# Kernel tuning notes

Hardware: AMD Instinct MI355X
Metric: run time of the kernel (lower is better)

The kernel has to match this reference:

```python
import jax, jax.numpy as jnp
import numpy as np

DIM = 256
NUM_HEADS = 8
HEAD_DIM = DIM // NUM_HEADS          # 32
KEY_DIM = int(HEAD_DIM * 0.5)        # 16
SCALE = KEY_DIM ** (-0.5)
QKV_OUT = DIM + 2 * KEY_DIM * NUM_HEADS  # 512
BN_EPS = 1e-3


def _bn(x, gamma, beta, mean, var):
    # inference-mode BatchNorm2d over channel axis 1 of NCHW
    inv = gamma / jnp.sqrt(var + BN_EPS)
    return x * inv[None, :, None, None] + (beta - mean * inv)[None, :, None, None]


def _conv1x1(x, w):
    # w: (O, C, 1, 1)
    return jnp.einsum('bchw,oc->bohw', x, w[:, :, 0, 0])


def _dwconv3x3(x, w):
    # depthwise 3x3, SAME padding; w: (C, 1, 3, 3)
    return jax.lax.conv_general_dilated(
        x, w, window_strides=(1, 1), padding='SAME',
        feature_group_count=x.shape[1],
        dimension_numbers=('NCHW', 'OIHW', 'NCHW'))


def setup_inputs() -> dict:
    key = jax.random.key(0)
    ks = jax.random.split(key, 16)
    B, C, H, W = 16, DIM, 32, 32
    inp = {
        'x': jax.random.normal(ks[0], (B, C, H, W), jnp.float32),
        'qkv_w': jax.random.normal(ks[1], (QKV_OUT, DIM, 1, 1), jnp.float32) * (1.0 / np.sqrt(DIM)),
        'qkv_gamma': jnp.ones((QKV_OUT,), jnp.float32),
        'qkv_beta': jnp.zeros((QKV_OUT,), jnp.float32),
        'qkv_mean': jax.random.normal(ks[2], (QKV_OUT,), jnp.float32) * 0.1,
        'qkv_var': jax.random.uniform(ks[3], (QKV_OUT,), jnp.float32, 0.5, 1.5),
        'pe_w': jax.random.normal(ks[4], (DIM, 1, 3, 3), jnp.float32) * (1.0 / 3.0),
        'pe_gamma': jnp.ones((DIM,), jnp.float32),
        'pe_beta': jnp.zeros((DIM,), jnp.float32),
        'pe_mean': jax.random.normal(ks[5], (DIM,), jnp.float32) * 0.1,
        'pe_var': jax.random.uniform(ks[6], (DIM,), jnp.float32, 0.5, 1.5),
        'proj_w': jax.random.normal(ks[7], (DIM, DIM, 1, 1), jnp.float32) * (1.0 / np.sqrt(DIM)),
        'proj_gamma': jnp.ones((DIM,), jnp.float32),
        'proj_beta': jnp.zeros((DIM,), jnp.float32),
        'proj_mean': jax.random.normal(ks[8], (DIM,), jnp.float32) * 0.1,
        'proj_var': jax.random.uniform(ks[9], (DIM,), jnp.float32, 0.5, 1.5),
    }
    return inp


def reference(x, qkv_w, qkv_gamma, qkv_beta, qkv_mean, qkv_var,
              pe_w, pe_gamma, pe_beta, pe_mean, pe_var,
              proj_w, proj_gamma, proj_beta, proj_mean, proj_var):
    B, C, H, W = x.shape
    N = H * W
    # qkv: 1x1 conv + BN (act=False)
    qkv = _bn(_conv1x1(x, qkv_w), qkv_gamma, qkv_beta, qkv_mean, qkv_var)
    qkv = qkv.reshape(B, NUM_HEADS, 2 * KEY_DIM + HEAD_DIM, N)
    q = qkv[:, :, :KEY_DIM]                          # (B, h, kd, N)
    k = qkv[:, :, KEY_DIM:2 * KEY_DIM]               # (B, h, kd, N)
    v = qkv[:, :, 2 * KEY_DIM:]                      # (B, h, hd, N)
    # attn = (q^T @ k) * scale, softmax over last dim
    attn = jnp.einsum('bhdn,bhdm->bhnm', q, k) * SCALE   # (B, h, N, N)
    attn = jax.nn.softmax(attn, axis=-1)
    # v @ attn^T
    v_attn = jnp.einsum('bhdn,bhmn->bhdm', v, attn)      # (B, h, hd, N)
    v_attn = v_attn.reshape(B, C, H, W)
    v_reshaped = v.reshape(B, C, H, W)
    pos_enc = _bn(_dwconv3x3(v_reshaped, pe_w), pe_gamma, pe_beta, pe_mean, pe_var)
    out = v_attn + pos_enc
    out = _bn(_conv1x1(out, proj_w), proj_gamma, proj_beta, proj_mean, proj_var)
    return out
```

## Files before the change

kernel.cpp:

```cpp
#include <hip/hip_runtime.h>

#define B_ 16
#define C_ 256
#define N_ 1024
#define NH 8
#define HD 32
#define KD 16
#define QKV_OUT_ 512
#define BN_EPS 1e-3f
#define SCALE2_ (0.25f * 1.44269504088896f)

typedef __attribute__((ext_vector_type(8))) short short8;
typedef __attribute__((ext_vector_type(16))) float float16;

__device__ inline unsigned short f2bf(float f) {
  unsigned int u = __float_as_uint(f);
  return (unsigned short)((u + 0x7FFF + ((u >> 16) & 1)) >> 16);
}
__device__ inline float bf2f(unsigned short s) {
  return __uint_as_float(((unsigned int)s) << 16);
}
__device__ inline float16 zero16() {
  float16 z;
  #pragma unroll
  for (int i = 0; i < 16; ++i) z[i] = 0.f;
  return z;
}
__device__ inline unsigned int pack_bf16_trunc(float a, float b) {
  return __builtin_amdgcn_perm(__float_as_uint(b), __float_as_uint(a), 0x07060302u);
}
__device__ inline unsigned int pack_bf16_rne(float a, float b) {
  return (unsigned int)f2bf(a) | ((unsigned int)f2bf(b) << 16);
}
__device__ inline float fast_exp2(float x) {
#if __has_builtin(__builtin_amdgcn_exp2f)
  return __builtin_amdgcn_exp2f(x);
#else
  return exp2f(x);
#endif
}

__global__ __launch_bounds__(256) void fold_weights(
    const float* __restrict__ qkv_w, const float* __restrict__ qg,
    const float* __restrict__ qb, const float* __restrict__ qm,
    const float* __restrict__ qv,
    const float* __restrict__ proj_w, const float* __restrict__ pg,
    const float* __restrict__ pb, const float* __restrict__ pm,
    const float* __restrict__ pv,
    unsigned short* __restrict__ wq, float* __restrict__ biasq,
    unsigned short* __restrict__ wp, float* __restrict__ biasp)
{
  const int o = blockIdx.x, c = threadIdx.x;
  if (o < QKV_OUT_) {
    float inv = qg[o] * rsqrtf(qv[o] + BN_EPS);
    wq[o * C_ + c] = f2bf(qkv_w[o * C_ + c] * inv);
    if (c == 0) biasq[o] = qb[o] - qm[o] * inv;
  } else {
    int oo = o - QKV_OUT_;
    float inv = pg[oo] * rsqrtf(pv[oo] + BN_EPS);
    wp[oo * C_ + c] = f2bf(proj_w[oo * C_ + c] * inv);
    if (c == 0) biasp[oo] = pb[oo] - pm[oo] * inv;
  }
}

__global__ __launch_bounds__(256) void transpose_x(
    const float* __restrict__ x, unsigned short* __restrict__ xT)
{
  __shared__ float t[64][69];
  const int tid = threadIdx.x;
  const int nt = blockIdx.x, ct = blockIdx.y, b = blockIdx.z;
  const int n0 = nt * 64, c0 = ct * 64;

  #pragma unroll
  for (int it = 0; it < 4; ++it) {
    int cl = it * 16 + (tid >> 4);
    int nl = (tid & 15) * 4;
    float4 v = *(const float4*)(x + ((size_t)b * C_ + c0 + cl) * N_ + n0 + nl);
    t[cl][nl + 0] = v.x; t[cl][nl + 1] = v.y;
    t[cl][nl + 2] = v.z; t[cl][nl + 3] = v.w;
  }
  __syncthreads();

  const int nr = tid >> 2, cseg = (tid & 3) * 16;
  unsigned int pk[8];
  #pragma unroll
  for (int q = 0; q < 8; ++q)
    pk[q] = pack_bf16_rne(t[cseg + 2 * q][nr], t[cseg + 2 * q + 1][nr]);
  unsigned short* row = xT + ((size_t)b * N_ + n0 + nr) * C_ + c0 + cseg;
  *(uint4*)(row)     = make_uint4(pk[0], pk[1], pk[2], pk[3]);
  *(uint4*)(row + 8) = make_uint4(pk[4], pk[5], pk[6], pk[7]);
}

template <int MODE>
__global__ __launch_bounds__(256) void gemm_tiled(
    const unsigned short* __restrict__ inT, const unsigned short* __restrict__ wfold,
    const float* __restrict__ bias,
    unsigned short* __restrict__ qkT, unsigned short* __restrict__ vbuf,
    float* __restrict__ outf)
{
  __shared__ __align__(16) unsigned short wa[128 * 72];
  __shared__ __align__(16) unsigned short xb[128 * 72];
  const int tid = threadIdx.x;
  const int wave = tid >> 6, lane = tid & 63, l31 = lane & 31, lh = lane >> 5;
  const int wm = wave & 1, wn = wave >> 1;
  const int n0g = blockIdx.x * 128;
  const int o0 = blockIdx.y * 128;
  const int b = n0g >> 10, nloc = n0g & 1023;

  const int sr = tid >> 3, sseg = (tid & 7) * 8;

  float16 acc[2][2];
  #pragma unroll
  for (int i = 0; i < 2; ++i)
    #pragma unroll
    for (int j = 0; j < 2; ++j) acc[i][j] = zero16();

  for (int kc = 0; kc < 4; ++kc) {
    __syncthreads();
    #pragma unroll
    for (int rr = 0; rr < 4; ++rr) {
      int r = rr * 32 + sr;
      *(uint4*)&wa[r * 72 + sseg] =
          *(const uint4*)(wfold + (size_t)(o0 + r) * C_ + kc * 64 + sseg);
      *(uint4*)&xb[r * 72 + sseg] =
          *(const uint4*)(inT + (size_t)(n0g + r) * C_ + kc * 64 + sseg);
    }
    __syncthreads();

    #pragma unroll
    for (int ks = 0; ks < 4; ++ks) {
      const int ko = ks * 16 + lh * 8;
      short8 a0 = *(const short8*)&wa[(wm * 64 + l31) * 72 + ko];
      short8 a1 = *(const short8*)&wa[(wm * 64 + 32 + l31) * 72 + ko];
      short8 b0 = *(const short8*)&xb[(wn * 64 + l31) * 72 + ko];
      short8 b1 = *(const short8*)&xb[(wn * 64 + 32 + l31) * 72 + ko];
      acc[0][0] = __builtin_amdgcn_mfma_f32_32x32x16_bf16(a0, b0, acc[0][0], 0, 0, 0);
      acc[0][1] = __builtin_amdgcn_mfma_f32_32x32x16_bf16(a0, b1, acc[0][1], 0, 0, 0);
      acc[1][0] = __builtin_amdgcn_mfma_f32_32x32x16_bf16(a1, b0, acc[1][0], 0, 0, 0);
      acc[1][1] = __builtin_amdgcn_mfma_f32_32x32x16_bf16(a1, b1, acc[1][1], 0, 0, 0);
    }
  }

  if constexpr (MODE == 0) {
    const int h = (o0 >> 6) + wm * 2 ;
    const int hh = (o0 >> 6) + wm;
    (void)h;
    #pragma unroll
    for (int bn = 0; bn < 2; ++bn) {
      int n = nloc + wn * 64 + bn * 32 + l31;
      unsigned short* row = qkT + (((size_t)b * NH + hh) * N_ + n) * 32;
      #pragma unroll
      for (int qd = 0; qd < 4; ++qd) {
        int cc0 = 8 * qd + 4 * lh;
        ushort4 rv;
        rv.x = f2bf(acc[0][bn][4 * qd + 0] + bias[hh * 64 + cc0 + 0]);
        rv.y = f2bf(acc[0][bn][4 * qd + 1] + bias[hh * 64 + cc0 + 1]);
        rv.z = f2bf(acc[0][bn][4 * qd + 2] + bias[hh * 64 + cc0 + 2]);
        rv.w = f2bf(acc[0][bn][4 * qd + 3] + bias[hh * 64 + cc0 + 3]);
        *(ushort4*)(row + cc0) = rv;
      }
    }
    #pragma unroll
    for (int r = 0; r < 16; ++r) {
      int d = (r & 3) + 8 * (r >> 2) + 4 * lh;
      float bo = bias[hh * 64 + 32 + d];
      unsigned short* vrow =
          vbuf + ((size_t)b * C_ + hh * 32 + d) * N_ + nloc + wn * 64 + l31;
      #pragma unroll
      for (int bn = 0; bn < 2; ++bn)
        vrow[bn * 32] = f2bf(acc[1][bn][r] + bo);
    }
  } else {
    #pragma unroll
    for (int am = 0; am < 2; ++am) {
      #pragma unroll
      for (int r = 0; r < 16; ++r) {
        int o = o0 + wm * 64 + am * 32 + (r & 3) + 8 * (r >> 2) + 4 * lh;
        float bo = bias[o];
        float* orow = outf + ((size_t)b * C_ + o) * N_ + nloc + wn * 64 + l31;
        #pragma unroll
        for (int bn = 0; bn < 2; ++bn)
          orow[bn * 32] = acc[am][bn][r] + bo;
      }
    }
  }
}

__global__ __launch_bounds__(256) void dwconv_bn(
    const unsigned short* __restrict__ vbuf, const float* __restrict__ pw,
    const float* __restrict__ gamma, const float* __restrict__ beta,
    const float* __restrict__ mean, const float* __restrict__ var,
    float* __restrict__ posenc)
{
  __shared__ float t[34][34];
  const int c = blockIdx.x, b = blockIdx.y;
  const int tid = threadIdx.x;
  const unsigned short* vp = vbuf + ((size_t)b * C_ + c) * N_;

  #pragma unroll
  for (int r = 0; r < 4; ++r) {
    int idx = r * 256 + tid;
    t[(idx >> 5) + 1][(idx & 31) + 1] = bf2f(vp[idx]);
  }
  if (tid < 34) {
    t[0][tid] = 0.f; t[33][tid] = 0.f;
    t[tid][0] = 0.f; t[tid][33] = 0.f;
  }
  __syncthreads();

  float w9[9];
  #pragma unroll
  for (int i = 0; i < 9; ++i) w9[i] = pw[c * 9 + i];
  float inv = gamma[c] * rsqrtf(var[c] + BN_EPS);
  float add = beta[c] - mean[c] * inv;

  float* op = posenc + ((size_t)b * C_ + c) * N_;
  #pragma unroll
  for (int r = 0; r < 4; ++r) {
    int idx = r * 256 + tid;
    int y = idx >> 5, x = idx & 31;
    float s = 0.f;
    #pragma unroll
    for (int dy = 0; dy < 3; ++dy)
      #pragma unroll
      for (int dx = 0; dx < 3; ++dx)
        s += t[y + dy][x + dx] * w9[dy * 3 + dx];
    op[idx] = s * inv + add;
  }
}

__global__ __launch_bounds__(256) void attn_mfma(
    const unsigned short* __restrict__ qkT, const unsigned short* __restrict__ vbuf,
    const float* __restrict__ posenc, unsigned short* __restrict__ vattnT)
{
  __shared__ __align__(16) unsigned short k_lds[2][128 * 24];
  __shared__ __align__(16) unsigned short v_lds[2][32 * 136];

  const int tid = threadIdx.x;
  const int wave = tid >> 6, lane = tid & 63;
  const int l31 = lane & 31, lh = lane >> 5;
  const int h = blockIdx.y, b = blockIdx.z;
  const int qbase = blockIdx.x * 128 + wave * 32;

  const unsigned short* qkb = qkT + ((size_t)b * NH + h) * N_ * 32;
  const unsigned short* vhead = vbuf + ((size_t)b * C_ + h * HD) * N_;

  const int skey = tid >> 1, shalf = tid & 1;
  const int svd = tid >> 4, svseg = tid & 15;

  short8 qf;
  {
    const unsigned short* qr = qkb + (size_t)(qbase + l31) * 32 + lh * 8;
    #pragma unroll
    for (int j = 0; j < 8; ++j)
      qf[j] = (short)f2bf(bf2f(qr[j]) * SCALE2_);
  }

  {
    *(uint4*)&k_lds[0][skey * 24 + shalf * 8] =
        *(const uint4*)(qkb + (size_t)skey * 32 + 16 + shalf * 8);
    #pragma unroll
    for (int r = 0; r < 2; ++r) {
      int d = r * 16 + svd;
      *(uint4*)&v_lds[0][d * 136 + svseg * 8] =
          *(const uint4*)(vhead + (size_t)d * N_ + svseg * 8);
    }
  }
  __syncthreads();

  float16 oacc = zero16();
  float ls[8];
  #pragma unroll
  for (int q = 0; q < 8; ++q) ls[q] = 0.f;

  for (int c = 0; c < 8; ++c) {
    const int buf = c & 1;
    if (c < 7) {
      int kc = (c + 1) * 128;
      *(uint4*)&k_lds[buf ^ 1][skey * 24 + shalf * 8] =
          *(const uint4*)(qkb + (size_t)(kc + skey) * 32 + 16 + shalf * 8);
      #pragma unroll
      for (int r = 0; r < 2; ++r) {
        int d = r * 16 + svd;
        *(uint4*)&v_lds[buf ^ 1][d * 136 + svseg * 8] =
            *(const uint4*)(vhead + (size_t)d * N_ + kc + svseg * 8);
      }
    }

    #pragma unroll
    for (int t = 0; t < 4; ++t) {
      const int key0 = t * 32;
      short8 kf = *(const short8*)&k_lds[buf][(key0 + l31) * 24 + lh * 8];
      float16 st = __builtin_amdgcn_mfma_f32_32x32x16_bf16(kf, qf, zero16(), 0, 0, 0);

      unsigned int u[8];
      #pragma unroll
      for (int q = 0; q < 8; ++q) {
        float pe = fast_exp2(st[2 * q]);
        float po = fast_exp2(st[2 * q + 1]);
        ls[q] += pe + po;
        u[q] = pack_bf16_trunc(pe, po);
      }
      unsigned int e[8];
      #pragma unroll
      for (int q = 0; q < 8; ++q)
        e[q] = (unsigned int)__shfl_xor((int)u[q], 32, 64);

      #pragma unroll
      for (int f = 0; f < 2; ++f) {
        union { unsigned int w[4]; short8 s; } bf;
        int q0 = f * 4;
        bf.w[0] = lh ? e[q0 + 2] : u[q0 + 0];
        bf.w[1] = lh ? e[q0 + 3] : u[q0 + 1];
        bf.w[2] = lh ? u[q0 + 2] : e[q0 + 0];
        bf.w[3] = lh ? u[q0 + 3] : e[q0 + 1];
        short8 vf = *(const short8*)&v_lds[buf][l31 * 136 + key0 + f * 16 + lh * 8];
        oacc = __builtin_amdgcn_mfma_f32_32x32x16_bf16(vf, bf.s, oacc, 0, 0, 0);
      }
    }
    __syncthreads();
  }

  float lsum = ((ls[0] + ls[1]) + (ls[2] + ls[3])) + ((ls[4] + ls[5]) + (ls[6] + ls[7]));
  lsum += __shfl_xor(lsum, 32, 64);
  float linv = 1.f / lsum;

  const int token = qbase + l31;
  float val[16];
  #pragma unroll
  for (int r = 0; r < 16; ++r) {
    int d = (r & 3) + 8 * (r >> 2) + 4 * lh;
    val[r] = oacc[r] * linv + posenc[((size_t)b * C_ + h * HD + d) * N_ + token];
  }
  unsigned int u[8];
  #pragma unroll
  for (int m = 0; m < 8; ++m) u[m] = pack_bf16_rne(val[2 * m], val[2 * m + 1]);
  unsigned int e[8];
  #pragma unroll
  for (int m = 0; m < 8; ++m) e[m] = (unsigned int)__shfl_xor((int)u[m], 32, 64);

  unsigned short* row = vattnT + ((size_t)b * N_ + token) * C_ + h * HD + lh * 16;
  uint4 w0, w1;
  if (lh == 0) {
    w0 = make_uint4(u[0], u[1], e[0], e[1]);
    w1 = make_uint4(u[2], u[3], e[2], e[3]);
  } else {
    w0 = make_uint4(e[4], e[5], u[4], u[5]);
    w1 = make_uint4(e[6], e[7], u[6], u[7]);
  }
  *(uint4*)(row)     = w0;
  *(uint4*)(row + 8) = w1;
}

extern "C" void kernel_launch(void* const* d_in, const int* in_sizes, int n_in,
                              void* d_out, int out_size, void* d_ws, size_t ws_size,
                              hipStream_t stream) {
  const float* x          = (const float*)d_in[0];
  const float* qkv_w      = (const float*)d_in[1];
  const float* qkv_gamma  = (const float*)d_in[2];
  const float* qkv_beta   = (const float*)d_in[3];
  const float* qkv_mean   = (const float*)d_in[4];
  const float* qkv_var    = (const float*)d_in[5];
  const float* pe_w       = (const float*)d_in[6];
  const float* pe_gamma   = (const float*)d_in[7];
  const float* pe_beta    = (const float*)d_in[8];
  const float* pe_mean    = (const float*)d_in[9];
  const float* pe_var     = (const float*)d_in[10];
  const float* proj_w     = (const float*)d_in[11];
  const float* proj_gamma = (const float*)d_in[12];
  const float* proj_beta  = (const float*)d_in[13];
  const float* proj_mean  = (const float*)d_in[14];
  const float* proj_var   = (const float*)d_in[15];
  float* out = (float*)d_out;

  char* ws = (char*)d_ws;
  unsigned short* qkT = (unsigned short*)ws;
  ws += (size_t)B_ * NH * N_ * 32 * sizeof(unsigned short);
  unsigned short* vbuf = (unsigned short*)ws;
  ws += (size_t)B_ * C_ * N_ * sizeof(unsigned short);
  unsigned short* xT = (unsigned short*)ws;
  ws += (size_t)B_ * N_ * C_ * sizeof(unsigned short);
  unsigned short* vattnT = (unsigned short*)ws;
  ws += (size_t)B_ * N_ * C_ * sizeof(unsigned short);
  float* posenc = (float*)ws;
  ws += (size_t)B_ * C_ * N_ * sizeof(float);
  unsigned short* wq = (unsigned short*)ws;
  ws += (size_t)QKV_OUT_ * C_ * sizeof(unsigned short);
  unsigned short* wp = (unsigned short*)ws;
  ws += (size_t)C_ * C_ * sizeof(unsigned short);
  float* biasq = (float*)ws; ws += QKV_OUT_ * sizeof(float);
  float* biasp = (float*)ws;

  fold_weights<<<dim3(QKV_OUT_ + C_), 256, 0, stream>>>(
      qkv_w, qkv_gamma, qkv_beta, qkv_mean, qkv_var,
      proj_w, proj_gamma, proj_beta, proj_mean, proj_var,
      wq, biasq, wp, biasp);
  transpose_x<<<dim3(16, 4, 16), 256, 0, stream>>>(x, xT);

  gemm_tiled<0><<<dim3(128, 4), 256, 0, stream>>>(
      xT, wq, biasq, qkT, vbuf, nullptr);

  dwconv_bn<<<dim3(C_, B_), 256, 0, stream>>>(
      vbuf, pe_w, pe_gamma, pe_beta, pe_mean, pe_var, posenc);

  attn_mfma<<<dim3(8, NH, B_), 256, 0, stream>>>(qkT, vbuf, posenc, vattnT);

  gemm_tiled<1><<<dim3(128, 2), 256, 0, stream>>>(
      vattnT, wp, biasp, nullptr, nullptr, out);
}
```

Before: 177.3 us.

## Double-buffer GEMM, widen attention query tile, fold scale into weights, bf16 posenc

Several changes land together. The attention softmax scale is folded into the q weights and bias, which removes the per-load rescale of q. The GEMM gets a double-buffered LDS pipeline with 32-wide K chunks, and attention now processes 64 queries per wave so each K/V fragment is reused twice, with grid.x halved. Lane exchanges switch to permlane32_swap, and the positional-encoding buffer is stored in bf16 to halve its traffic. The risks are higher register pressure from the two accumulators per wave, fewer attention blocks (512), and bf16 rounding of posenc.

```diff
diff --git a/kernel.cpp b/kernel.cpp
--- a/kernel.cpp
+++ b/kernel.cpp
@@ -38,6 +38,31 @@
 #else
   return exp2f(x);
 #endif
+}
+__device__ inline void pl32(unsigned int& a, unsigned int& b) {
+#if __has_builtin(__builtin_amdgcn_permlane32_swap)
+  typedef __attribute__((ext_vector_type(2))) int int2v;
+  int2v r = __builtin_amdgcn_permlane32_swap((int)a, (int)b, false, false);
+  a = (unsigned int)r[0];
+  b = (unsigned int)r[1];
+#else
+  unsigned int ea = (unsigned int)__shfl_xor((int)a, 32, 64);
+  unsigned int eb = (unsigned int)__shfl_xor((int)b, 32, 64);
+  bool hi = (threadIdx.x & 32) != 0;
+  unsigned int an = hi ? eb : a;
+  unsigned int bn = hi ? b : ea;
+  a = an; b = bn;
+#endif
+}
+__device__ inline short8 lds_frag(const unsigned short* p) {
+  union { uint2 u[2]; short8 s; } r;
+  r.u[0] = *(const uint2*)p;
+  r.u[1] = *(const uint2*)(p + 4);
+  return r.s;
+}
+__device__ inline void lds_store16(unsigned short* p, uint4 v) {
+  *(uint2*)p = make_uint2(v.x, v.y);
+  *(uint2*)(p + 4) = make_uint2(v.z, v.w);
 }
 
 __global__ __launch_bounds__(256) void fold_weights(
@@ -52,9 +77,10 @@
 {
   const int o = blockIdx.x, c = threadIdx.x;
   if (o < QKV_OUT_) {
-    float inv = qg[o] * rsqrtf(qv[o] + BN_EPS);
+    float s = ((o & 63) < 16) ? SCALE2_ : 1.f;
+    float inv = qg[o] * rsqrtf(qv[o] + BN_EPS) * s;
     wq[o * C_ + c] = f2bf(qkv_w[o * C_ + c] * inv);
-    if (c == 0) biasq[o] = qb[o] - qm[o] * inv;
+    if (c == 0) biasq[o] = qb[o] * s - qm[o] * inv;
   } else {
     int oo = o - QKV_OUT_;
     float inv = pg[oo] * rsqrtf(pv[oo] + BN_EPS);
@@ -98,8 +124,9 @@
     unsigned short* __restrict__ qkT, unsigned short* __restrict__ vbuf,
     float* __restrict__ outf)
 {
-  __shared__ __align__(16) unsigned short wa[128 * 72];
-  __shared__ __align__(16) unsigned short xb[128 * 72];
+  constexpr int STR = 44;
+  __shared__ __align__(8) unsigned short wa[2][128 * STR];
+  __shared__ __align__(8) unsigned short xb[2][128 * STR];
   const int tid = threadIdx.x;
   const int wave = tid >> 6, lane = tid & 63, l31 = lane & 31, lh = lane >> 5;
   const int wm = wave & 1, wn = wave >> 1;
@@ -107,7 +134,8 @@
   const int o0 = blockIdx.y * 128;
   const int b = n0g >> 10, nloc = n0g & 1023;
 
-  const int sr = tid >> 3, sseg = (tid & 7) * 8;
+  const int r0 = tid >> 2, oc0 = (tid & 3) * 8;
+  const int r1 = (tid + 256) >> 2, oc1 = oc0;
 
   float16 acc[2][2];
   #pragma unroll
@@ -115,36 +143,47 @@
     #pragma unroll
     for (int j = 0; j < 2; ++j) acc[i][j] = zero16();
 
-  for (int kc = 0; kc < 4; ++kc) {
-    __syncthreads();
-    #pragma unroll
-    for (int rr = 0; rr < 4; ++rr) {
-      int r = rr * 32 + sr;
-      *(uint4*)&wa[r * 72 + sseg] =
-          *(const uint4*)(wfold + (size_t)(o0 + r) * C_ + kc * 64 + sseg);
-      *(uint4*)&xb[r * 72 + sseg] =
-          *(const uint4*)(inT + (size_t)(n0g + r) * C_ + kc * 64 + sseg);
-    }
-    __syncthreads();
-
-    #pragma unroll
-    for (int ks = 0; ks < 4; ++ks) {
+  uint4 ga0, ga1, gb0, gb1;
+  #define LOADK(kc)                                                          \
+    ga0 = *(const uint4*)(wfold + (size_t)(o0 + r0) * C_ + (kc) * 32 + oc0); \
+    ga1 = *(const uint4*)(wfold + (size_t)(o0 + r1) * C_ + (kc) * 32 + oc1); \
+    gb0 = *(const uint4*)(inT + (size_t)(n0g + r0) * C_ + (kc) * 32 + oc0);  \
+    gb1 = *(const uint4*)(inT + (size_t)(n0g + r1) * C_ + (kc) * 32 + oc1);
+  #define STOREK(bufi)                                   \
+    lds_store16(&wa[bufi][r0 * STR + oc0], ga0);         \
+    lds_store16(&wa[bufi][r1 * STR + oc1], ga1);         \
+    lds_store16(&xb[bufi][r0 * STR + oc0], gb0);         \
+    lds_store16(&xb[bufi][r1 * STR + oc1], gb1);
+
+  LOADK(0);
+  STOREK(0);
+  __syncthreads();
+
+  for (int kc = 0; kc < 8; ++kc) {
+    const int buf = kc & 1;
+    if (kc < 7) { LOADK(kc + 1); }
+
+    #pragma unroll
+    for (int ks = 0; ks < 2; ++ks) {
       const int ko = ks * 16 + lh * 8;
-      short8 a0 = *(const short8*)&wa[(wm * 64 + l31) * 72 + ko];
-      short8 a1 = *(const short8*)&wa[(wm * 64 + 32 + l31) * 72 + ko];
-      short8 b0 = *(const short8*)&xb[(wn * 64 + l31) * 72 + ko];
-      short8 b1 = *(const short8*)&xb[(wn * 64 + 32 + l31) * 72 + ko];
+      short8 a0 = lds_frag(&wa[buf][(wm * 64 + l31) * STR + ko]);
+      short8 a1 = lds_frag(&wa[buf][(wm * 64 + 32 + l31) * STR + ko]);
+      short8 b0 = lds_frag(&xb[buf][(wn * 64 + l31) * STR + ko]);
+      short8 b1 = lds_frag(&xb[buf][(wn * 64 + 32 + l31) * STR + ko]);
       acc[0][0] = __builtin_amdgcn_mfma_f32_32x32x16_bf16(a0, b0, acc[0][0], 0, 0, 0);
       acc[0][1] = __builtin_amdgcn_mfma_f32_32x32x16_bf16(a0, b1, acc[0][1], 0, 0, 0);
       acc[1][0] = __builtin_amdgcn_mfma_f32_32x32x16_bf16(a1, b0, acc[1][0], 0, 0, 0);
       acc[1][1] = __builtin_amdgcn_mfma_f32_32x32x16_bf16(a1, b1, acc[1][1], 0, 0, 0);
     }
-  }
+
+    if (kc < 7) { STOREK(buf ^ 1); }
+    __syncthreads();
+  }
+  #undef LOADK
+  #undef STOREK
 
   if constexpr (MODE == 0) {
-    const int h = (o0 >> 6) + wm * 2 ;
     const int hh = (o0 >> 6) + wm;
-    (void)h;
     #pragma unroll
     for (int bn = 0; bn < 2; ++bn) {
       int n = nloc + wn * 64 + bn * 32 + l31;
@@ -190,7 +229,7 @@
     const unsigned short* __restrict__ vbuf, const float* __restrict__ pw,
     const float* __restrict__ gamma, const float* __restrict__ beta,
     const float* __restrict__ mean, const float* __restrict__ var,
-    float* __restrict__ posenc)
+    unsigned short* __restrict__ posb)
 {
   __shared__ float t[34][34];
   const int c = blockIdx.x, b = blockIdx.y;
@@ -214,7 +253,7 @@
   float inv = gamma[c] * rsqrtf(var[c] + BN_EPS);
   float add = beta[c] - mean[c] * inv;
 
-  float* op = posenc + ((size_t)b * C_ + c) * N_;
+  unsigned short* op = posb + ((size_t)b * C_ + c) * N_;
   #pragma unroll
   for (int r = 0; r < 4; ++r) {
     int idx = r * 256 + tid;
@@ -225,131 +264,129 @@
       #pragma unroll
       for (int dx = 0; dx < 3; ++dx)
         s += t[y + dy][x + dx] * w9[dy * 3 + dx];
-    op[idx] = s * inv + add;
+    op[idx] = f2bf(s * inv + add);
   }
 }
 
 __global__ __launch_bounds__(256) void attn_mfma(
     const unsigned short* __restrict__ qkT, const unsigned short* __restrict__ vbuf,
-    const float* __restrict__ posenc, unsigned short* __restrict__ vattnT)
+    const unsigned short* __restrict__ posb, unsigned short* __restrict__ vattnT)
 {
-  __shared__ __align__(16) unsigned short k_lds[2][128 * 24];
-  __shared__ __align__(16) unsigned short v_lds[2][32 * 136];
+  __shared__ __align__(8) unsigned short k_lds[2][128 * 28];
+  __shared__ __align__(8) unsigned short v_lds[2][32 * 140];
 
   const int tid = threadIdx.x;
   const int wave = tid >> 6, lane = tid & 63;
   const int l31 = lane & 31, lh = lane >> 5;
   const int h = blockIdx.y, b = blockIdx.z;
-  const int qbase = blockIdx.x * 128 + wave * 32;
+  const int qbase = blockIdx.x * 256 + wave * 64;
 
   const unsigned short* qkb = qkT + ((size_t)b * NH + h) * N_ * 32;
   const unsigned short* vhead = vbuf + ((size_t)b * C_ + h * HD) * N_;
 
   const int skey = tid >> 1, shalf = tid & 1;
-  const int svd = tid >> 4, svseg = tid & 15;
-
-  short8 qf;
-  {
-    const unsigned short* qr = qkb + (size_t)(qbase + l31) * 32 + lh * 8;
-    #pragma unroll
-    for (int j = 0; j < 8; ++j)
-      qf[j] = (short)f2bf(bf2f(qr[j]) * SCALE2_);
-  }
-
-  {
-    *(uint4*)&k_lds[0][skey * 24 + shalf * 8] =
-        *(const uint4*)(qkb + (size_t)skey * 32 + 16 + shalf * 8);
-    #pragma unroll
-    for (int r = 0; r < 2; ++r) {
-      int d = r * 16 + svd;
-      *(uint4*)&v_lds[0][d * 136 + svseg * 8] =
-          *(const uint4*)(vhead + (size_t)d * N_ + svseg * 8);
-    }
-  }
+  const int svd = tid >> 3, svseg = tid & 7;
+
+  short8 qfA = lds_frag(qkb + (size_t)(qbase + l31) * 32 + lh * 8);
+  short8 qfB = lds_frag(qkb + (size_t)(qbase + 32 + l31) * 32 + lh * 8);
+
+  uint4 gk, gv0, gv1;
+  #define LOADC(kc)                                                             \
+    gk  = *(const uint4*)(qkb + (size_t)((kc) + skey) * 32 + 16 + shalf * 8);   \
+    gv0 = *(const uint4*)(vhead + (size_t)svd * N_ + (kc) + svseg * 16);        \
+    gv1 = *(const uint4*)(vhead + (size_t)svd * N_ + (kc) + svseg * 16 + 8);
+  #define STOREC(bufi)                                        \
+    lds_store16(&k_lds[bufi][skey * 28 + shalf * 8], gk);     \
+    lds_store16(&v_lds[bufi][svd * 140 + svseg * 16], gv0);   \
+    lds_store16(&v_lds[bufi][svd * 140 + svseg * 16 + 8], gv1);
+
+  LOADC(0);
+  STOREC(0);
   __syncthreads();
 
-  float16 oacc = zero16();
-  float ls[8];
-  #pragma unroll
-  for (int q = 0; q < 8; ++q) ls[q] = 0.f;
+  float16 oaccA = zero16(), oaccB = zero16();
+  float lsA[4] = {0.f, 0.f, 0.f, 0.f}, lsB[4] = {0.f, 0.f, 0.f, 0.f};
 
   for (int c = 0; c < 8; ++c) {
     const int buf = c & 1;
-    if (c < 7) {
-      int kc = (c + 1) * 128;
-      *(uint4*)&k_lds[buf ^ 1][skey * 24 + shalf * 8] =
-          *(const uint4*)(qkb + (size_t)(kc + skey) * 32 + 16 + shalf * 8);
-      #pragma unroll
-      for (int r = 0; r < 2; ++r) {
-        int d = r * 16 + svd;
-        *(uint4*)&v_lds[buf ^ 1][d * 136 + svseg * 8] =
-            *(const uint4*)(vhead + (size_t)d * N_ + kc + svseg * 8);
-      }
-    }
+    if (c < 7) { LOADC((c + 1) * 128); }
 
     #pragma unroll
     for (int t = 0; t < 4; ++t) {
       const int key0 = t * 32;
-      short8 kf = *(const short8*)&k_lds[buf][(key0 + l31) * 24 + lh * 8];
-      float16 st = __builtin_amdgcn_mfma_f32_32x32x16_bf16(kf, qf, zero16(), 0, 0, 0);
-
-      unsigned int u[8];
+      short8 kf = lds_frag(&k_lds[buf][(key0 + l31) * 28 + lh * 8]);
+      float16 stA = __builtin_amdgcn_mfma_f32_32x32x16_bf16(kf, qfA, zero16(), 0, 0, 0);
+      float16 stB = __builtin_amdgcn_mfma_f32_32x32x16_bf16(kf, qfB, zero16(), 0, 0, 0);
+
+      unsigned int uA[8], uB[8];
       #pragma unroll
       for (int q = 0; q < 8; ++q) {
-        float pe = fast_exp2(st[2 * q]);
-        float po = fast_exp2(st[2 * q + 1]);
-        ls[q] += pe + po;
-        u[q] = pack_bf16_trunc(pe, po);
+        float pe = fast_exp2(stA[2 * q]);
+        float po = fast_exp2(stA[2 * q + 1]);
+        lsA[q & 3] += pe + po;
+        uA[q] = pack_bf16_trunc(pe, po);
       }
-      unsigned int e[8];
-      #pragma unroll
-      for (int q = 0; q < 8; ++q)
-        e[q] = (unsigned int)__shfl_xor((int)u[q], 32, 64);
+      #pragma unroll
+      for (int q = 0; q < 8; ++q) {
+        float pe = fast_exp2(stB[2 * q]);
+        float po = fast_exp2(stB[2 * q + 1]);
+        lsB[q & 3] += pe + po;
+        uB[q] = pack_bf16_trunc(pe, po);
+      }
 
       #pragma unroll
       for (int f = 0; f < 2; ++f) {
-        union { unsigned int w[4]; short8 s; } bf;
-        int q0 = f * 4;
-        bf.w[0] = lh ? e[q0 + 2] : u[q0 + 0];
-        bf.w[1] = lh ? e[q0 + 3] : u[q0 + 1];
-        bf.w[2] = lh ? u[q0 + 2] : e[q0 + 0];
-        bf.w[3] = lh ? u[q0 + 3] : e[q0 + 1];
-        short8 vf = *(const short8*)&v_lds[buf][l31 * 136 + key0 + f * 16 + lh * 8];
-        oacc = __builtin_amdgcn_mfma_f32_32x32x16_bf16(vf, bf.s, oacc, 0, 0, 0);
+        short8 vf = lds_frag(&v_lds[buf][l31 * 140 + key0 + f * 16 + lh * 8]);
+        const int q0 = f * 4;
+        {
+          unsigned int a0 = uA[q0], a2 = uA[q0 + 2]; pl32(a0, a2);
+          unsigned int a1 = uA[q0 + 1], a3 = uA[q0 + 3]; pl32(a1, a3);
+          union { unsigned int w[4]; short8 s; } bf;
+          bf.w[0] = a0; bf.w[1] = a1; bf.w[2] = a2; bf.w[3] = a3;
+          oaccA = __builtin_amdgcn_mfma_f32_32x32x16_bf16(vf, bf.s, oaccA, 0, 0, 0);
+        }
+        {
+          unsigned int a0 = uB[q0], a2 = uB[q0 + 2]; pl32(a0, a2);
+          unsigned int a1 = uB[q0 + 1], a3 = uB[q0 + 3]; pl32(a1, a3);
+          union { unsigned int w[4]; short8 s; } bf;
+          bf.w[0] = a0; bf.w[1] = a1; bf.w[2] = a2; bf.w[3] = a3;
+          oaccB = __builtin_amdgcn_mfma_f32_32x32x16_bf16(vf, bf.s, oaccB, 0, 0, 0);
+        }
       }
     }
+
+    if (c < 7) { STOREC(buf ^ 1); }
     __syncthreads();
   }
-
-  float lsum = ((ls[0] + ls[1]) + (ls[2] + ls[3])) + ((ls[4] + ls[5]) + (ls[6] + ls[7]));
-  lsum += __shfl_xor(lsum, 32, 64);
-  float linv = 1.f / lsum;
-
-  const int token = qbase + l31;
-  float val[16];
-  #pragma unroll
-  for (int r = 0; r < 16; ++r) {
-    int d = (r & 3) + 8 * (r >> 2) + 4 * lh;
-    val[r] = oacc[r] * linv + posenc[((size_t)b * C_ + h * HD + d) * N_ + token];
-  }
-  unsigned int u[8];
-  #pragma unroll
-  for (int m = 0; m < 8; ++m) u[m] = pack_bf16_rne(val[2 * m], val[2 * m + 1]);
-  unsigned int e[8];
-  #pragma unroll
-  for (int m = 0; m < 8; ++m) e[m] = (unsigned int)__shfl_xor((int)u[m], 32, 64);
-
-  unsigned short* row = vattnT + ((size_t)b * N_ + token) * C_ + h * HD + lh * 16;
-  uint4 w0, w1;
-  if (lh == 0) {
-    w0 = make_uint4(u[0], u[1], e[0], e[1]);
-    w1 = make_uint4(u[2], u[3], e[2], e[3]);
-  } else {
-    w0 = make_uint4(e[4], e[5], u[4], u[5]);
-    w1 = make_uint4(e[6], e[7], u[6], u[7]);
-  }
-  *(uint4*)(row)     = w0;
-  *(uint4*)(row + 8) = w1;
+  #undef LOADC
+  #undef STOREC
+
+  float lsumA = (lsA[0] + lsA[1]) + (lsA[2] + lsA[3]);
+  float lsumB = (lsB[0] + lsB[1]) + (lsB[2] + lsB[3]);
+  lsumA += __shfl_xor(lsumA, 32, 64);
+  lsumB += __shfl_xor(lsumB, 32, 64);
+  const float linvA = 1.f / lsumA, linvB = 1.f / lsumB;
+
+  #pragma unroll
+  for (int g = 0; g < 2; ++g) {
+    const float16& oacc = g ? oaccB : oaccA;
+    const float linv = g ? linvB : linvA;
+    const int token = qbase + g * 32 + l31;
+    float val[16];
+    #pragma unroll
+    for (int r = 0; r < 16; ++r) {
+      int d = (r & 3) + 8 * (r >> 2) + 4 * lh;
+      val[r] = oacc[r] * linv +
+               bf2f(posb[((size_t)b * C_ + h * HD + d) * N_ + token]);
+    }
+    unsigned int u[8];
+    #pragma unroll
+    for (int m = 0; m < 8; ++m) u[m] = pack_bf16_rne(val[2 * m], val[2 * m + 1]);
+    pl32(u[0], u[4]); pl32(u[1], u[5]); pl32(u[2], u[6]); pl32(u[3], u[7]);
+    unsigned short* row = vattnT + ((size_t)b * N_ + token) * C_ + h * HD + lh * 16;
+    *(uint4*)(row)     = make_uint4(u[0], u[1], u[4], u[5]);
+    *(uint4*)(row + 8) = make_uint4(u[2], u[3], u[6], u[7]);
+  }
 }
 
 extern "C" void kernel_launch(void* const* d_in, const int* in_sizes, int n_in,
@@ -382,8 +419,8 @@
   ws += (size_t)B_ * N_ * C_ * sizeof(unsigned short);
   unsigned short* vattnT = (unsigned short*)ws;
   ws += (size_t)B_ * N_ * C_ * sizeof(unsigned short);
-  float* posenc = (float*)ws;
-  ws += (size_t)B_ * C_ * N_ * sizeof(float);
+  unsigned short* posb = (unsigned short*)ws;
+  ws += (size_t)B_ * C_ * N_ * sizeof(unsigned short);
   unsigned short* wq = (unsigned short*)ws;
   ws += (size_t)QKV_OUT_ * C_ * sizeof(unsigned short);
   unsigned short* wp = (unsigned short*)ws;
@@ -401,9 +438,9 @@
       xT, wq, biasq, qkT, vbuf, nullptr);
 
   dwconv_bn<<<dim3(C_, B_), 256, 0, stream>>>(
-      vbuf, pe_w, pe_gamma, pe_beta, pe_mean, pe_var, posenc);
-
-  attn_mfma<<<dim3(8, NH, B_), 256, 0, stream>>>(qkT, vbuf, posenc, vattnT);
+      vbuf, pe_w, pe_gamma, pe_beta, pe_mean, pe_var, posb);
+
+  attn_mfma<<<dim3(4, NH, B_), 256, 0, stream>>>(qkT, vbuf, posb, vattnT);
 
   gemm_tiled<1><<<dim3(128, 2), 256, 0, stream>>>(
       vattnT, wp, biasp, nullptr, nullptr, out);
```

After: 161.3 us. 9.0% less time.
